# Kernel tuning notes

Measured on AMD Instinct MI355X. Metric: run time of the kernel, lower is better.

The kernel has to match this reference:

```python
import jax, jax.numpy as jnp
from jax import lax
import numpy as np

B, T, V, U = 64, 2048, 256, 256
BLANK = 0
NEG = jnp.float32(-1e30)


def setup_inputs() -> dict:
    key = jax.random.key(0)
    k1, k2, k3, k4 = jax.random.split(key, 4)
    logits = jax.random.normal(k1, (B, T, V), dtype=jnp.float32)
    targets = jax.random.randint(k2, (B, U), 1, V)               # labels 1..V-1 (0 = blank)
    targets_lengths = jax.random.randint(k3, (B,), U // 2, U + 1)
    logits_lengths = jax.random.randint(k4, (B,), T // 2, T + 1)
    return dict(logits=logits, targets=targets,
                logits_lengths=logits_lengths, targets_lengths=targets_lengths)


def _ctc_forced_alignment(logp, targets, logits_lengths, targets_lengths):
    """Viterbi forced alignment over the CTC extended state graph.
    Returns per-frame best-path labels, shape [B, T] (get_alignment_3d, is_ctc=True)."""
    Bs, Ts, _ = logp.shape
    Us = targets.shape[1]
    S = 2 * Us + 1
    s_idx = jnp.arange(S)
    # extended sequence: blank, t1, blank, t2, ..., blank
    lab_pos = jnp.minimum(s_idx // 2, Us - 1)
    ext = jnp.where((s_idx % 2 == 1)[None, :], jnp.take(targets, lab_pos, axis=1), BLANK)  # [B,S]
    # emission scores em[b,t,s] = logp[b,t,ext[b,s]]
    em = jnp.take_along_axis(logp, jnp.broadcast_to(ext[:, None, :], (Bs, Ts, S)), axis=2)

    valid = s_idx[None, :] < (2 * targets_lengths[:, None] + 1)              # [B,S]
    ext_m2 = jnp.pad(ext[:, :-2], ((0, 0), (2, 0)), constant_values=BLANK)
    skip_ok = (s_idx[None, :] >= 2) & ((s_idx % 2 == 1)[None, :]) & (ext != ext_m2)

    idx_blank = 2 * targets_lengths          # last blank state (S_b - 1)
    idx_label = 2 * targets_lengths - 1      # last label state (S_b - 2)

    alpha0 = jnp.where(valid & (s_idx[None, :] <= 1), em[:, 0, :], NEG)

    def pair_of(alpha):
        vb = jnp.take_along_axis(alpha, idx_blank[:, None], axis=1)
        vl = jnp.take_along_axis(alpha, idx_label[:, None], axis=1)
        return jnp.concatenate([vb, vl], axis=1)  # [B,2]

    def step(alpha, em_t):
        a1 = jnp.pad(alpha[:, :-1], ((0, 0), (1, 0)), constant_values=NEG)
        a2 = jnp.where(skip_ok, jnp.pad(alpha[:, :-2], ((0, 0), (2, 0)), constant_values=NEG), NEG)
        stacked = jnp.stack([alpha, a1, a2])     # [3,B,S]
        bp = jnp.argmax(stacked, axis=0).astype(jnp.int32)
        alpha_new = jnp.where(valid, jnp.max(stacked, axis=0) + em_t, NEG)
        return alpha_new, (bp, pair_of(alpha_new))

    _, (bps, pairs) = lax.scan(step, alpha0, jnp.moveaxis(em, 1, 0)[1:])
    bps = jnp.concatenate([jnp.zeros((1, Bs, S), jnp.int32), bps])            # [T,B,S]
    pairs = jnp.concatenate([pair_of(alpha0)[None], pairs])                   # [T,B,2]

    last_pair = pairs[logits_lengths - 1, jnp.arange(Bs)]                     # value at final valid frame
    end_state = jnp.where(last_pair[:, 0] >= last_pair[:, 1], idx_blank, idx_label).astype(jnp.int32)

    def back(s, inp):
        t, bp_t = inp
        label = jnp.take_along_axis(ext, s[:, None], axis=1)[:, 0]
        step_bp = jnp.take_along_axis(bp_t, s[:, None], axis=1)[:, 0]
        s_prev = jnp.where(t - 1 >= logits_lengths - 1, end_state, s - step_bp)
        return s_prev.astype(jnp.int32), label

    ts = jnp.arange(Ts - 1, -1, -1)
    _, labels_rev = lax.scan(back, end_state, (ts, bps[::-1]))
    return labels_rev[::-1].T  # [B,T] per-frame aligned target labels


def reference(logits, targets, logits_lengths, targets_lengths):
    logp = jax.nn.log_softmax(logits, axis=2)                                 # [B,T,V]
    aligned = lax.stop_gradient(
        _ctc_forced_alignment(logp, targets, logits_lengths, targets_lengths))
    nll = -jnp.take_along_axis(logp, aligned[:, :, None], axis=2)[..., 0]     # [B,T]
    mask = (jnp.arange(logp.shape[1])[None, :] < logits_lengths[:, None]).astype(logp.dtype)
    # reduce=True: mean over valid (unmasked) positions
    return jnp.sum(nll * mask) / jnp.sum(mask)
```

## Files before the change

### kernel.cpp

```cpp
#include <hip/hip_runtime.h>

#define NEGF -1e30f
typedef unsigned int uint32;

static constexpr int Bb = 64, Tt = 2048, Vv = 256, Uu = 256;

__device__ __forceinline__ unsigned short f2bf(float f) {
  uint32 u = __builtin_bit_cast(uint32, f);
  u += 0x7fffu + ((u >> 16) & 1u);
  return (unsigned short)(u >> 16);
}
__device__ __forceinline__ float bf2f_lo(uint32 p) { return __builtin_bit_cast(float, p << 16); }
__device__ __forceinline__ float bf2f_hi(uint32 p) { return __builtin_bit_cast(float, p & 0xffff0000u); }

__global__ __launch_bounds__(256) void gather_lse_kernel(
    const float* __restrict__ logits, const int* __restrict__ targets,
    const int* __restrict__ llen, float* __restrict__ acc,
    float* __restrict__ Ebs, unsigned short* __restrict__ E) {
  __shared__ __align__(16) float buf[4][8][Vv];
  __shared__ float wpart[4];
  const int b = blockIdx.x >> 5;
  const int c = blockIdx.x & 31;
  const int w = threadIdx.x >> 6;
  const int lane = threadIdx.x & 63;
  const int L = llen[b];
  const int4 lb = reinterpret_cast<const int4*>(targets + (b << 8))[lane];
  const float* __restrict__ lgb = logits + (size_t)b * (Tt * Vv);
  float lse_local = 0.f;
#pragma unroll
  for (int k = 0; k < 2; ++k) {
    const int tbase = (c << 6) + (k << 5) + w;
    if (tbase >= L) break;
    float4 v[8];
#pragma unroll
    for (int j = 0; j < 8; ++j)
      v[j] = reinterpret_cast<const float4*>(lgb + (size_t)(tbase + 4 * j) * Vv)[lane];
    float s[8];
#pragma unroll
    for (int j = 0; j < 8; ++j)
      s[j] = __expf(v[j].x) + __expf(v[j].y) + __expf(v[j].z) + __expf(v[j].w);
#pragma unroll
    for (int off = 32; off; off >>= 1) {
#pragma unroll
      for (int j = 0; j < 8; ++j) s[j] += __shfl_down(s[j], off);
    }
#pragma unroll
    for (int j = 0; j < 8; ++j)
      reinterpret_cast<float4*>(&buf[w][j][0])[lane] = v[j];
#pragma unroll
    for (int j = 0; j < 8; ++j) {
      const int t = tbase + 4 * j;
      const bool val = t < L;
      ushort4 o;
      o.x = f2bf(buf[w][j][lb.x]); o.y = f2bf(buf[w][j][lb.y]);
      o.z = f2bf(buf[w][j][lb.z]); o.w = f2bf(buf[w][j][lb.w]);
      if (val)
        reinterpret_cast<ushort4*>(E + ((size_t)((b << 11) + t)) * Vv)[lane] = o;
      if ((lane == 0) & val) {
        lse_local += __logf(s[j]);
        Ebs[(b << 11) + ((t == 0) ? 2047 : t - 1)] = v[j].x;
      }
    }
  }
  if (lane == 0) wpart[w] = lse_local;
  __syncthreads();
  if (threadIdx.x == 0)
    atomicAdd(acc, wpart[0] + wpart[1] + wpart[2] + wpart[3]);
}

#define PG 8
__global__ __launch_bounds__(128) void viterbi_kernel(
    const unsigned short* __restrict__ E, const float* __restrict__ Ebs,
    const int* __restrict__ targets, const int* __restrict__ llen,
    const int* __restrict__ tlen, float* __restrict__ acc) {
  __shared__ __align__(16) float LB[2048];
  __shared__ float Bt[520];
  const int b = blockIdx.x;
  const int lane = threadIdx.x & 63;
  const int wv = threadIdx.x >> 6;
  const int L = llen[b];
  const int tl = tlen[b];
  const int M = (L - 2) >> 1;
  const int4 lb = reinterpret_cast<const int4*>(targets + (b << 8))[lane];
  const uint2* __restrict__ Erow = reinterpret_cast<const uint2*>(E) + ((size_t)(b << 11) << 6);
  const float* __restrict__ Ebb = Ebs + (b << 11);

  {
    const float4* src = reinterpret_cast<const float4*>(Ebb);
    float4* dst = reinterpret_cast<float4*>(LB);
    for (int i = threadIdx.x; i < 512; i += 128) dst[i] = src[i];
  }
  __syncthreads();

  float a0 = NEGF, a1 = NEGF, a2 = NEGF, a3 = NEGF, a4 = NEGF,
        a5 = NEGF, a6 = NEGF, a7 = NEGF, a8 = NEGF;

  if (wv == 0) {
    const int prevw = __shfl_up(lb.w, 1);
    const bool sk0 = (lane != 0) && (lb.x != prevw);
    const bool sk1 = (lb.y != lb.x);
    const bool sk2 = (lb.z != lb.y);
    const bool sk3 = (lb.w != lb.z);
    if (lane == 0) {
      a0 = LB[2047];
      a1 = bf2f_lo((uint32)*reinterpret_cast<const unsigned short*>(E + ((size_t)(b << 11) << 8)));
    }
    uint2 pf[PG][4];
    float4 pb[PG];
    auto fetchf = [&](int slot, int k) {
      const int kk = (k > 511) ? 511 : k;
#pragma unroll
      for (int j = 0; j < 4; ++j) {
        int r = 1 + 4 * kk + j; r = (r > 2047) ? 2047 : r;
        pf[slot][j] = Erow[(size_t)(r << 6) + lane];
      }
      pb[slot] = reinterpret_cast<const float4*>(LB)[kk];
    };
    auto stepf = [&](uint2 em, float eb) {
      const float e0 = bf2f_lo(em.x), e1 = bf2f_hi(em.x);
      const float e2 = bf2f_lo(em.y), e3 = bf2f_hi(em.y);
      float am1 = __shfl_up(a7, 1);
      if (lane == 0) am1 = NEGF;
      const float x0 = fmaxf(a0, am1) + eb;
      const float x1 = fmaxf(fmaxf(a1, a0), sk0 ? am1 : NEGF) + e0;
      const float x2 = fmaxf(a2, a1) + eb;
      const float x3 = fmaxf(fmaxf(a3, a2), sk1 ? a1 : NEGF) + e1;
      const float x4 = fmaxf(a4, a3) + eb;
      const float x5 = fmaxf(fmaxf(a5, a4), sk2 ? a3 : NEGF) + e2;
      const float x6 = fmaxf(a6, a5) + eb;
      const float x7 = fmaxf(fmaxf(a7, a6), sk3 ? a5 : NEGF) + e3;
      const float x8 = fmaxf(a8, a7) + eb;
      a0 = x0; a1 = x1; a2 = x2; a3 = x3; a4 = x4; a5 = x5; a6 = x6; a7 = x7; a8 = x8;
    };
    const int n = M, Gf = n >> 2, remf = n & 3;
#pragma unroll
    for (int s = 0; s < PG; ++s) fetchf(s, s);
    __builtin_amdgcn_sched_barrier(0);
    int g = 0;
    while (g + PG <= Gf) {
#pragma unroll
      for (int s = 0; s < PG; ++s) {
#pragma unroll
        for (int j = 0; j < 4; ++j) stepf(pf[s][j], (&pb[s].x)[j]);
        fetchf(s, g + s + PG);
        __builtin_amdgcn_sched_barrier(0);
      }
      g += PG;
    }
    const int left = Gf - g;
#pragma unroll
    for (int s = 0; s < PG; ++s) {
      if (s < left) {
#pragma unroll
        for (int j = 0; j < 4; ++j) stepf(pf[s][j], (&pb[s].x)[j]);
      }
    }
#pragma unroll
    for (int s = 0; s < PG; ++s) {
      if (s == left) {
#pragma unroll
        for (int j = 0; j < 4; ++j)
          if (j < remf) stepf(pf[s][j], (&pb[s].x)[j]);
      }
    }
  } else {
    const int nlabx = __shfl_down(lb.x, 1);
    const bool kb0 = (lb.y != lb.x);
    const bool kb1 = (lb.z != lb.y);
    const bool kb2 = (lb.w != lb.z);
    const bool kb3 = (lane < 63) && (nlabx != lb.w);
    {
      const uint2 er = Erow[(size_t)((L - 1) << 6) + lane];
      const float e0 = bf2f_lo(er.x), e1 = bf2f_hi(er.x);
      const float e2 = bf2f_lo(er.y), e3 = bf2f_hi(er.y);
      const float blankL = LB[L - 2];
      const int s0 = 8 * lane, tb = 2 * tl, tm = 2 * tl - 1;
      a0 = (s0     == tb) ? blankL : NEGF;
      a1 = (s0 + 1 == tm) ? e0     : NEGF;
      a2 = (s0 + 2 == tb) ? blankL : NEGF;
      a3 = (s0 + 3 == tm) ? e1     : NEGF;
      a4 = (s0 + 4 == tb) ? blankL : NEGF;
      a5 = (s0 + 5 == tm) ? e2     : NEGF;
      a6 = (s0 + 6 == tb) ? blankL : NEGF;
      a7 = (s0 + 7 == tm) ? e3     : NEGF;
      a8 = ((lane == 63) && (tb == 512)) ? blankL : NEGF;
    }
    uint2 qf[PG][4];
    float qb[PG][4];
    auto fetchb = [&](int slot, int k) {
#pragma unroll
      for (int j = 0; j < 4; ++j) {
        int r = L - 2 - 4 * k - j; r = (r < 1) ? 1 : r;
        qf[slot][j] = Erow[(size_t)(r << 6) + lane];
        int ix = r - 1;
        qb[slot][j] = LB[ix];
      }
    };
    auto stepb = [&](uint2 em, float eb) {
      const float e0 = bf2f_lo(em.x), e1 = bf2f_hi(em.x);
      const float e2 = bf2f_lo(em.y), e3 = bf2f_hi(em.y);
      float bn0 = __shfl_down(a0, 1);
      float bn1 = __shfl_down(a1, 1);
      bn0 = (lane == 63) ? a8 : bn0;
      const float y0 = fmaxf(a0, a1) + eb;
      const float y1 = fmaxf(fmaxf(a1, a2), kb0 ? a3 : NEGF) + e0;
      const float y2 = fmaxf(a2, a3) + eb;
      const float y3 = fmaxf(fmaxf(a3, a4), kb1 ? a5 : NEGF) + e1;
      const float y4 = fmaxf(a4, a5) + eb;
      const float y5 = fmaxf(fmaxf(a5, a6), kb2 ? a7 : NEGF) + e2;
      const float y6 = fmaxf(a6, a7) + eb;
      const float y7 = fmaxf(fmaxf(a7, bn0), kb3 ? bn1 : NEGF) + e3;
      const float y8 = a8 + eb;
      a0 = y0; a1 = y1; a2 = y2; a3 = y3; a4 = y4; a5 = y5; a6 = y6; a7 = y7; a8 = y8;
    };
    const int n = L - 2 - M, Gb = n >> 2, remb = n & 3;
#pragma unroll
    for (int s = 0; s < PG; ++s) fetchb(s, s);
    __builtin_amdgcn_sched_barrier(0);
    int g = 0;
    while (g + PG <= Gb) {
#pragma unroll
      for (int s = 0; s < PG; ++s) {
#pragma unroll
        for (int j = 0; j < 4; ++j) stepb(qf[s][j], qb[s][j]);
        fetchb(s, g + s + PG);
        __builtin_amdgcn_sched_barrier(0);
      }
      g += PG;
    }
    const int left = Gb - g;
#pragma unroll
    for (int s = 0; s < PG; ++s) {
      if (s < left) {
#pragma unroll
        for (int j = 0; j < 4; ++j) stepb(qf[s][j], qb[s][j]);
      }
    }
#pragma unroll
    for (int s = 0; s < PG; ++s) {
      if (s == left) {
#pragma unroll
        for (int j = 0; j < 4; ++j)
          if (j < remb) stepb(qf[s][j], qb[s][j]);
      }
    }
    Bt[8 * lane + 0] = a0; Bt[8 * lane + 1] = a1;
    Bt[8 * lane + 2] = a2; Bt[8 * lane + 3] = a3;
    Bt[8 * lane + 4] = a4; Bt[8 * lane + 5] = a5;
    Bt[8 * lane + 6] = a6; Bt[8 * lane + 7] = a7;
    if (lane == 63) Bt[512] = a8;
    if (lane == 0) { Bt[513] = NEGF; Bt[514] = NEGF; }
  }
  __syncthreads();
  if (wv == 0) {
    const int nlabx = __shfl_down(lb.x, 1);
    const bool kb0 = (lb.y != lb.x);
    const bool kb1 = (lb.z != lb.y);
    const bool kb2 = (lb.w != lb.z);
    const bool kb3 = (lane < 63) && (nlabx != lb.w);
    const int s0 = 8 * lane;
    float best;
    best =             a0 + fmaxf(Bt[s0],     Bt[s0 + 1]);
    best = fmaxf(best, a1 + fmaxf(fmaxf(Bt[s0 + 1], Bt[s0 + 2]), kb0 ? Bt[s0 + 3] : NEGF));
    best = fmaxf(best, a2 + fmaxf(Bt[s0 + 2], Bt[s0 + 3]));
    best = fmaxf(best, a3 + fmaxf(fmaxf(Bt[s0 + 3], Bt[s0 + 4]), kb1 ? Bt[s0 + 5] : NEGF));
    best = fmaxf(best, a4 + fmaxf(Bt[s0 + 4], Bt[s0 + 5]));
    best = fmaxf(best, a5 + fmaxf(fmaxf(Bt[s0 + 5], Bt[s0 + 6]), kb2 ? Bt[s0 + 7] : NEGF));
    best = fmaxf(best, a6 + fmaxf(Bt[s0 + 6], Bt[s0 + 7]));
    best = fmaxf(best, a7 + fmaxf(fmaxf(Bt[s0 + 7], Bt[s0 + 8]), kb3 ? Bt[s0 + 9] : NEGF));
    best = fmaxf(best, a8 + Bt[512]);
#pragma unroll
    for (int off = 32; off; off >>= 1) best = fmaxf(best, __shfl_down(best, off));
    if (lane == 0) atomicAdd(acc, -best);
  }
}

__global__ __launch_bounds__(64) void finalize_kernel(
    const int* __restrict__ llen, const float* __restrict__ acc,
    float* __restrict__ out) {
  int Lsum = llen[threadIdx.x];
#pragma unroll
  for (int off = 32; off; off >>= 1) Lsum += __shfl_down(Lsum, off);
  if (threadIdx.x == 0) out[0] = acc[0] / (float)Lsum;
}

extern "C" void kernel_launch(void* const* d_in, const int* in_sizes, int n_in,
                              void* d_out, int out_size, void* d_ws, size_t ws_size,
                              hipStream_t stream) {
  const float* logits  = (const float*)d_in[0];
  const int*   targets = (const int*)d_in[1];
  const int*   llen    = (const int*)d_in[2];
  const int*   tlen    = (const int*)d_in[3];
  float* out = (float*)d_out;

  float*          acc = (float*)d_ws;
  float*          Ebs = (float*)((char*)d_ws + 4096);
  unsigned short* E   = (unsigned short*)((char*)d_ws + (1u << 20));

  hipMemsetAsync(acc, 0, 16, stream);
  gather_lse_kernel<<<Bb * 32, 256, 0, stream>>>(logits, targets, llen, acc, Ebs, E);
  viterbi_kernel<<<Bb, 128, 0, stream>>>(E, Ebs, targets, llen, tlen, acc);
  finalize_kernel<<<1, 64, 0, stream>>>(llen, acc, out);
}
```

Before: 287.8 us.

## Replace per-step cross-lane shuffles with LDS halo exchange every four steps

The forward and backward Viterbi sweeps no longer do a wavefront shuffle each time step to get the neighbouring lane's boundary state. Each lane now keeps a redundant copy of its neighbour's 8 states and advances it locally with a shrinking halo (catch1..3), using the neighbour's emissions loaded from an offset address. Neighbour state is exchanged through LDS once every four steps. This removes the per-step DPP/shuffle latency from the serial dependency chain, at the cost of extra redundant ALU work, doubled emission loads and more registers, so the prefetch depth drops from 8 to 6.

Result: slower. 356.1 us (+23.7%).

```diff
diff --git a/kernel.cpp b/kernel.cpp
--- a/kernel.cpp
+++ b/kernel.cpp
@@ -68,13 +68,15 @@
     atomicAdd(acc, wpart[0] + wpart[1] + wpart[2] + wpart[3]);
 }
 
-#define PG 8
+#define PG 6
 __global__ __launch_bounds__(128) void viterbi_kernel(
     const unsigned short* __restrict__ E, const float* __restrict__ Ebs,
     const int* __restrict__ targets, const int* __restrict__ llen,
     const int* __restrict__ tlen, float* __restrict__ acc) {
   __shared__ __align__(16) float LB[2048];
   __shared__ float Bt[520];
+  __shared__ __align__(16) float4 Hf[130];
+  __shared__ __align__(16) float4 Hb[130];
   const int b = blockIdx.x;
   const int lane = threadIdx.x & 63;
   const int wv = threadIdx.x >> 6;
@@ -94,6 +96,8 @@
 
   float a0 = NEGF, a1 = NEGF, a2 = NEGF, a3 = NEGF, a4 = NEGF,
         a5 = NEGF, a6 = NEGF, a7 = NEGF, a8 = NEGF;
+  float h0 = NEGF, h1 = NEGF, h2 = NEGF, h3 = NEGF,
+        h4 = NEGF, h5 = NEGF, h6 = NEGF, h7 = NEGF;
 
   if (wv == 0) {
     const int prevw = __shfl_up(lb.w, 1);
@@ -101,22 +105,100 @@
     const bool sk1 = (lb.y != lb.x);
     const bool sk2 = (lb.z != lb.y);
     const bool sk3 = (lb.w != lb.z);
+    const bool bh1 = __shfl_up((int)sk1, 1) != 0;
+    const bool bh2 = __shfl_up((int)sk2, 1) != 0;
+    const bool bh3 = __shfl_up((int)sk3, 1) != 0;
     if (lane == 0) {
       a0 = LB[2047];
       a1 = bf2f_lo((uint32)*reinterpret_cast<const unsigned short*>(E + ((size_t)(b << 11) << 8)));
-    }
-    uint2 pf[PG][4];
+      Hf[0] = make_float4(NEGF, NEGF, NEGF, NEGF);
+      Hf[1] = make_float4(NEGF, NEGF, NEGF, NEGF);
+    }
+    uint2 po[PG][4], pn[PG][4];
     float4 pb[PG];
     auto fetchf = [&](int slot, int k) {
       const int kk = (k > 511) ? 511 : k;
 #pragma unroll
       for (int j = 0; j < 4; ++j) {
         int r = 1 + 4 * kk + j; r = (r > 2047) ? 2047 : r;
-        pf[slot][j] = Erow[(size_t)(r << 6) + lane];
+        po[slot][j] = Erow[(size_t)(r << 6) + lane];
+        pn[slot][j] = reinterpret_cast<const uint2*>(
+            (const char*)Erow + ((size_t)(r << 6) + lane) * 8 - 8)[0];
       }
       pb[slot] = reinterpret_cast<const float4*>(LB)[kk];
     };
+    auto refreshf = [&]() {
+      Hf[2 * lane + 2] = make_float4(a0, a1, a2, a3);
+      Hf[2 * lane + 3] = make_float4(a4, a5, a6, a7);
+      const float4 v0 = Hf[2 * lane];
+      const float4 v1 = Hf[2 * lane + 1];
+      h0 = v0.x; h1 = v0.y; h2 = v0.z; h3 = v0.w;
+      h4 = v1.x; h5 = v1.y; h6 = v1.z; h7 = v1.w;
+    };
     auto stepf = [&](uint2 em, float eb) {
+      const float e0 = bf2f_lo(em.x), e1 = bf2f_hi(em.x);
+      const float e2 = bf2f_lo(em.y), e3 = bf2f_hi(em.y);
+      const float am1 = h7;
+      const float x0 = fmaxf(a0, am1) + eb;
+      const float x1 = fmaxf(fmaxf(a1, a0), sk0 ? am1 : NEGF) + e0;
+      const float x2 = fmaxf(a2, a1) + eb;
+      const float x3 = fmaxf(fmaxf(a3, a2), sk1 ? a1 : NEGF) + e1;
+      const float x4 = fmaxf(a4, a3) + eb;
+      const float x5 = fmaxf(fmaxf(a5, a4), sk2 ? a3 : NEGF) + e2;
+      const float x6 = fmaxf(a6, a5) + eb;
+      const float x7 = fmaxf(fmaxf(a7, a6), sk3 ? a5 : NEGF) + e3;
+      const float x8 = fmaxf(a8, a7) + eb;
+      a0 = x0; a1 = x1; a2 = x2; a3 = x3; a4 = x4; a5 = x5; a6 = x6; a7 = x7; a8 = x8;
+    };
+    auto catch1 = [&](uint2 nem, float eb) {
+      const float ne1 = bf2f_hi(nem.x), ne2 = bf2f_lo(nem.y), ne3 = bf2f_hi(nem.y);
+      const float t3 = fmaxf(fmaxf(h3, h2), bh1 ? h1 : NEGF) + ne1;
+      const float t4 = fmaxf(h4, h3) + eb;
+      const float t5 = fmaxf(fmaxf(h5, h4), bh2 ? h3 : NEGF) + ne2;
+      const float t6 = fmaxf(h6, h5) + eb;
+      const float t7 = fmaxf(fmaxf(h7, h6), bh3 ? h5 : NEGF) + ne3;
+      h3 = t3; h4 = t4; h5 = t5; h6 = t6; h7 = t7;
+    };
+    auto catch2 = [&](uint2 nem, float eb) {
+      const float ne2 = bf2f_lo(nem.y), ne3 = bf2f_hi(nem.y);
+      const float t5 = fmaxf(fmaxf(h5, h4), bh2 ? h3 : NEGF) + ne2;
+      const float t6 = fmaxf(h6, h5) + eb;
+      const float t7 = fmaxf(fmaxf(h7, h6), bh3 ? h5 : NEGF) + ne3;
+      h5 = t5; h6 = t6; h7 = t7;
+    };
+    auto catch3 = [&](uint2 nem) {
+      const float ne3 = bf2f_hi(nem.y);
+      h7 = fmaxf(fmaxf(h7, h6), bh3 ? h5 : NEGF) + ne3;
+    };
+    auto do_group = [&](int s) {
+      stepf(po[s][0], pb[s].x);  catch1(pn[s][0], pb[s].x);
+      stepf(po[s][1], pb[s].y);  catch2(pn[s][1], pb[s].y);
+      stepf(po[s][2], pb[s].z);  catch3(pn[s][2]);
+      stepf(po[s][3], pb[s].w);  refreshf();
+    };
+    const int n = M, G = n >> 2, rem = n & 3;
+    refreshf();
+#pragma unroll
+    for (int s = 0; s < PG; ++s) fetchf(s, s);
+    __builtin_amdgcn_sched_barrier(0);
+    int g = 0;
+    while (g + PG <= G) {
+#pragma unroll
+      for (int s = 0; s < PG; ++s) {
+        do_group(s);
+        fetchf(s, g + s + PG);
+        __builtin_amdgcn_sched_barrier(0);
+      }
+      g += PG;
+    }
+    const int left = G - g;
+#pragma unroll
+    for (int s = 0; s < PG; ++s)
+      if (s < left) do_group(s);
+    for (int i = 0; i < rem; ++i) {
+      const int r = 1 + 4 * G + i;
+      const uint2 em = Erow[(size_t)(r << 6) + lane];
+      const float eb = LB[r - 1];
       const float e0 = bf2f_lo(em.x), e1 = bf2f_hi(em.x);
       const float e2 = bf2f_lo(em.y), e3 = bf2f_hi(em.y);
       float am1 = __shfl_up(a7, 1);
@@ -131,37 +213,6 @@
       const float x7 = fmaxf(fmaxf(a7, a6), sk3 ? a5 : NEGF) + e3;
       const float x8 = fmaxf(a8, a7) + eb;
       a0 = x0; a1 = x1; a2 = x2; a3 = x3; a4 = x4; a5 = x5; a6 = x6; a7 = x7; a8 = x8;
-    };
-    const int n = M, Gf = n >> 2, remf = n & 3;
-#pragma unroll
-    for (int s = 0; s < PG; ++s) fetchf(s, s);
-    __builtin_amdgcn_sched_barrier(0);
-    int g = 0;
-    while (g + PG <= Gf) {
-#pragma unroll
-      for (int s = 0; s < PG; ++s) {
-#pragma unroll
-        for (int j = 0; j < 4; ++j) stepf(pf[s][j], (&pb[s].x)[j]);
-        fetchf(s, g + s + PG);
-        __builtin_amdgcn_sched_barrier(0);
-      }
-      g += PG;
-    }
-    const int left = Gf - g;
-#pragma unroll
-    for (int s = 0; s < PG; ++s) {
-      if (s < left) {
-#pragma unroll
-        for (int j = 0; j < 4; ++j) stepf(pf[s][j], (&pb[s].x)[j]);
-      }
-    }
-#pragma unroll
-    for (int s = 0; s < PG; ++s) {
-      if (s == left) {
-#pragma unroll
-        for (int j = 0; j < 4; ++j)
-          if (j < remf) stepf(pf[s][j], (&pb[s].x)[j]);
-      }
     }
   } else {
     const int nlabx = __shfl_down(lb.x, 1);
@@ -169,6 +220,9 @@
     const bool kb1 = (lb.z != lb.y);
     const bool kb2 = (lb.w != lb.z);
     const bool kb3 = (lane < 63) && (nlabx != lb.w);
+    const bool gh0 = __shfl_down((int)kb0, 1) != 0;
+    const bool gh1 = __shfl_down((int)kb1, 1) != 0;
+    const bool gh2 = __shfl_down((int)kb2, 1) != 0;
     {
       const uint2 er = Erow[(size_t)((L - 1) << 6) + lane];
       const float e0 = bf2f_lo(er.x), e1 = bf2f_hi(er.x);
@@ -184,19 +238,96 @@
       a6 = (s0 + 6 == tb) ? blankL : NEGF;
       a7 = (s0 + 7 == tm) ? e3     : NEGF;
       a8 = ((lane == 63) && (tb == 512)) ? blankL : NEGF;
-    }
-    uint2 qf[PG][4];
-    float qb[PG][4];
+      if (lane == 63) Hb[129] = make_float4(NEGF, NEGF, NEGF, NEGF);
+    }
+    uint2 po[PG][4], pn[PG][4];
+    float pq[PG][4];
     auto fetchb = [&](int slot, int k) {
 #pragma unroll
       for (int j = 0; j < 4; ++j) {
         int r = L - 2 - 4 * k - j; r = (r < 1) ? 1 : r;
-        qf[slot][j] = Erow[(size_t)(r << 6) + lane];
-        int ix = r - 1;
-        qb[slot][j] = LB[ix];
+        po[slot][j] = Erow[(size_t)(r << 6) + lane];
+        pn[slot][j] = reinterpret_cast<const uint2*>(
+            (const char*)Erow + ((size_t)(r << 6) + lane) * 8 + 8)[0];
+        pq[slot][j] = LB[r - 1];
       }
     };
+    auto refreshb = [&]() {
+      Hb[2 * lane]     = make_float4(a0, a1, a2, a3);
+      Hb[2 * lane + 1] = make_float4(a4, a5, a6, a7);
+      if (lane == 63) Hb[128] = make_float4(a8, NEGF, NEGF, NEGF);
+      const float4 v0 = Hb[2 * lane + 2];
+      const float4 v1 = Hb[2 * lane + 3];
+      h0 = v0.x; h1 = v0.y; h2 = v0.z; h3 = v0.w;
+      h4 = v1.x; h5 = v1.y; h6 = v1.z; h7 = v1.w;
+    };
     auto stepb = [&](uint2 em, float eb) {
+      const float e0 = bf2f_lo(em.x), e1 = bf2f_hi(em.x);
+      const float e2 = bf2f_lo(em.y), e3 = bf2f_hi(em.y);
+      const float y0 = fmaxf(a0, a1) + eb;
+      const float y1 = fmaxf(fmaxf(a1, a2), kb0 ? a3 : NEGF) + e0;
+      const float y2 = fmaxf(a2, a3) + eb;
+      const float y3 = fmaxf(fmaxf(a3, a4), kb1 ? a5 : NEGF) + e1;
+      const float y4 = fmaxf(a4, a5) + eb;
+      const float y5 = fmaxf(fmaxf(a5, a6), kb2 ? a7 : NEGF) + e2;
+      const float y6 = fmaxf(a6, a7) + eb;
+      const float y7 = fmaxf(fmaxf(a7, h0), kb3 ? h1 : NEGF) + e3;
+      const float y8 = a8 + eb;
+      a0 = y0; a1 = y1; a2 = y2; a3 = y3; a4 = y4; a5 = y5; a6 = y6; a7 = y7; a8 = y8;
+    };
+    auto catch1 = [&](uint2 nem, float eb) {
+      const float ne0 = bf2f_lo(nem.x), ne1 = bf2f_hi(nem.x), ne2 = bf2f_lo(nem.y);
+      const float t0 = fmaxf(h0, h1) + eb;
+      const float t1 = fmaxf(fmaxf(h1, h2), gh0 ? h3 : NEGF) + ne0;
+      const float t2 = fmaxf(h2, h3) + eb;
+      const float t3 = fmaxf(fmaxf(h3, h4), gh1 ? h5 : NEGF) + ne1;
+      const float t4 = fmaxf(h4, h5) + eb;
+      const float t5 = fmaxf(fmaxf(h5, h6), gh2 ? h7 : NEGF) + ne2;
+      h0 = t0; h1 = t1; h2 = t2; h3 = t3; h4 = t4; h5 = t5;
+    };
+    auto catch2 = [&](uint2 nem, float eb) {
+      const float ne0 = bf2f_lo(nem.x), ne1 = bf2f_hi(nem.x);
+      const float t0 = fmaxf(h0, h1) + eb;
+      const float t1 = fmaxf(fmaxf(h1, h2), gh0 ? h3 : NEGF) + ne0;
+      const float t2 = fmaxf(h2, h3) + eb;
+      const float t3 = fmaxf(fmaxf(h3, h4), gh1 ? h5 : NEGF) + ne1;
+      h0 = t0; h1 = t1; h2 = t2; h3 = t3;
+    };
+    auto catch3 = [&](uint2 nem, float eb) {
+      const float ne0 = bf2f_lo(nem.x);
+      const float t0 = fmaxf(h0, h1) + eb;
+      const float t1 = fmaxf(fmaxf(h1, h2), gh0 ? h3 : NEGF) + ne0;
+      h0 = t0; h1 = t1;
+    };
+    auto do_group = [&](int s) {
+      stepb(po[s][0], pq[s][0]);  catch1(pn[s][0], pq[s][0]);
+      stepb(po[s][1], pq[s][1]);  catch2(pn[s][1], pq[s][1]);
+      stepb(po[s][2], pq[s][2]);  catch3(pn[s][2], pq[s][2]);
+      stepb(po[s][3], pq[s][3]);  refreshb();
+    };
+    const int n = L - 2 - M, G = n >> 2, rem = n & 3;
+    refreshb();
+#pragma unroll
+    for (int s = 0; s < PG; ++s) fetchb(s, s);
+    __builtin_amdgcn_sched_barrier(0);
+    int g = 0;
+    while (g + PG <= G) {
+#pragma unroll
+      for (int s = 0; s < PG; ++s) {
+        do_group(s);
+        fetchb(s, g + s + PG);
+        __builtin_amdgcn_sched_barrier(0);
+      }
+      g += PG;
+    }
+    const int left = G - g;
+#pragma unroll
+    for (int s = 0; s < PG; ++s)
+      if (s < left) do_group(s);
+    for (int i = 0; i < rem; ++i) {
+      const int r = L - 2 - 4 * G - i;
+      const uint2 em = Erow[(size_t)(r << 6) + lane];
+      const float eb = LB[r - 1];
       const float e0 = bf2f_lo(em.x), e1 = bf2f_hi(em.x);
       const float e2 = bf2f_lo(em.y), e3 = bf2f_hi(em.y);
       float bn0 = __shfl_down(a0, 1);
@@ -212,37 +343,6 @@
       const float y7 = fmaxf(fmaxf(a7, bn0), kb3 ? bn1 : NEGF) + e3;
       const float y8 = a8 + eb;
       a0 = y0; a1 = y1; a2 = y2; a3 = y3; a4 = y4; a5 = y5; a6 = y6; a7 = y7; a8 = y8;
-    };
-    const int n = L - 2 - M, Gb = n >> 2, remb = n & 3;
-#pragma unroll
-    for (int s = 0; s < PG; ++s) fetchb(s, s);
-    __builtin_amdgcn_sched_barrier(0);
-    int g = 0;
-    while (g + PG <= Gb) {
-#pragma unroll
-      for (int s = 0; s < PG; ++s) {
-#pragma unroll
-        for (int j = 0; j < 4; ++j) stepb(qf[s][j], qb[s][j]);
-        fetchb(s, g + s + PG);
-        __builtin_amdgcn_sched_barrier(0);
-      }
-      g += PG;
-    }
-    const int left = Gb - g;
-#pragma unroll
-    for (int s = 0; s < PG; ++s) {
-      if (s < left) {
-#pragma unroll
-        for (int j = 0; j < 4; ++j) stepb(qf[s][j], qb[s][j]);
-      }
-    }
-#pragma unroll
-    for (int s = 0; s < PG; ++s) {
-      if (s == left) {
-#pragma unroll
-        for (int j = 0; j < 4; ++j)
-          if (j < remb) stepb(qf[s][j], qb[s][j]);
-      }
     }
     Bt[8 * lane + 0] = a0; Bt[8 * lane + 1] = a1;
     Bt[8 * lane + 2] = a2; Bt[8 * lane + 3] = a3;
```
